# Optimization experiments

Measured on AMD Instinct MI355X. Metric: run time of the kernel, lower is better.

The kernel has to match this reference:

```python
import jax, jax.numpy as jnp
import numpy as np

K = 8192   # codebook_size
D = 256    # latent_dim
COMMITMENT_COST = 0.25


def setup_inputs() -> dict:
    key = jax.random.key(0)
    kx, kw = jax.random.split(key)
    x = jax.random.normal(kx, (8, 4096, D), dtype=jnp.float32)
    # nn.init.uniform_(weight, -1/K, 1/K)
    weight = jax.random.uniform(kw, (K, D), dtype=jnp.float32,
                                minval=-1.0 / K, maxval=1.0 / K)
    return {"x": x, "weight": weight}


def reference(x, weight):
    sg = jax.lax.stop_gradient
    orig_shape = x.shape
    x_flat = x.reshape(-1, D)                      # [N, D]
    # squared euclidean distances; argmin identical to cdist argmin
    x_sq = jnp.sum(x_flat * x_flat, axis=-1, keepdims=True)      # [N, 1]
    w_sq = jnp.sum(weight * weight, axis=-1)                     # [K]
    dist2 = x_sq - 2.0 * (x_flat @ weight.T) + w_sq              # [N, K]
    indices = jnp.argmin(dist2, axis=1)                          # [N]
    quantized = jnp.take(weight, indices, axis=0).reshape(orig_shape)
    # eval / non-EMA branch of the torch module
    commitment_loss = jnp.mean((x - sg(quantized)) ** 2) * COMMITMENT_COST
    codebook_loss = jnp.mean((quantized - sg(x)) ** 2)
    total = commitment_loss + codebook_loss
    # straight-through estimator
    quantized_st = x + sg(quantized - x)
    indices_out = indices.reshape(orig_shape[:-1])
    return quantized_st, indices_out, commitment_loss, codebook_loss, total
```

## Files before the change

### kernel.cpp

```cpp
#include <hip/hip_runtime.h>

#define K_CB   8192
#define D_DIM  256
#define N_ROWS 32768
#define Q_ELEMS (N_ROWS * D_DIM)

#define M_FLAG 1.3e-4f
#define M_CAND 1.3e-4f
#define CAP    16

typedef __bf16 bf16x8 __attribute__((ext_vector_type(8)));
typedef float  f32x16 __attribute__((ext_vector_type(16)));

#define ASYNC_COPY16(gp, lp)                                              \
    __builtin_amdgcn_global_load_lds(                                     \
        (const __attribute__((address_space(1))) unsigned int*)(gp),      \
        (__attribute__((address_space(3))) unsigned int*)(lp), 16, 0, 0)


__device__ inline ushort f2bf(float f) {
    unsigned u = __float_as_uint(f);
    unsigned r = u + 0x7FFFu + ((u >> 16) & 1u);
    return (ushort)(r >> 16);
}

__device__ inline uint4 pack8(float4 a, float4 b) {
    uint4 o;
    o.x = (unsigned)f2bf(a.x) | ((unsigned)f2bf(a.y) << 16);
    o.y = (unsigned)f2bf(a.z) | ((unsigned)f2bf(a.w) << 16);
    o.z = (unsigned)f2bf(b.x) | ((unsigned)f2bf(b.y) << 16);
    o.w = (unsigned)f2bf(b.z) | ((unsigned)f2bf(b.w) << 16);
    return o;
}

__global__ void wsq_wbf_kernel(const float* __restrict__ w, float* __restrict__ wsq,
                               ushort* __restrict__ wbf) {
    int wave = threadIdx.x >> 6, lane = threadIdx.x & 63;
    int row = blockIdx.x * 4 + wave;
    float4 v = reinterpret_cast<const float4*>(w)[(size_t)row * 64 + lane];
    uint2 o;
    o.x = (unsigned)f2bf(-2.0f * v.x) | ((unsigned)f2bf(-2.0f * v.y) << 16);
    o.y = (unsigned)f2bf(-2.0f * v.z) | ((unsigned)f2bf(-2.0f * v.w) << 16);
    int c = row & 127, tile = row >> 7;
    int s = lane >> 1, hq = lane & 1;
    size_t dst = (size_t)tile * 65536 + (size_t)c * 512 + (size_t)((s ^ (c & 7)) * 16) + hq * 8;
    *reinterpret_cast<uint2*>((char*)wbf + dst) = o;
    double sq = (double)v.x * v.x + (double)v.y * v.y + (double)v.z * v.z + (double)v.w * v.w;
    #pragma unroll
    for (int off = 32; off > 0; off >>= 1) sq += __shfl_down(sq, off, 64);
    if (lane == 0) wsq[row] = (float)sq;
}

__global__ void sqx_kernel(const float* __restrict__ m, float* __restrict__ out) {
    int wave = threadIdx.x >> 6, lane = threadIdx.x & 63;
    int row = blockIdx.x * 4 + wave;
    float4 v = reinterpret_cast<const float4*>(m)[(size_t)row * 64 + lane];
    double s = (double)v.x * v.x + (double)v.y * v.y + (double)v.z * v.z + (double)v.w * v.w;
    #pragma unroll
    for (int off = 32; off > 0; off >>= 1) s += __shfl_down(s, off, 64);
    if (lane == 0) out[row] = (float)s;
}

__global__ __launch_bounds__(256, 2) void pass1_kernel(
        const float* __restrict__ x, const ushort* __restrict__ wbf,
        const float* __restrict__ wsq, float* __restrict__ idx_out,
        float* __restrict__ rowmin, int* __restrict__ flags,
        unsigned* __restrict__ flag_count, int* __restrict__ hard_flags,
        unsigned* __restrict__ hard_count, int* __restrict__ candcnt,
        int* __restrict__ cands) {
    __shared__ __align__(16) ushort wt[128 * 256];

    const int t = threadIdx.x;
    const int lane = t & 63, ln31 = lane & 31, h = lane >> 5;
    const int wv = t >> 6, rs = wv & 1, cs = wv >> 1;
    const int r0 = blockIdx.x * 64;

    const int arow = r0 + rs * 32 + ln31;
    const float4* xr = reinterpret_cast<const float4*>(x) + (size_t)arow * 64;
    bf16x8 afr[16];
    #pragma unroll
    for (int kk = 0; kk < 16; ++kk)
        afr[kk] = __builtin_bit_cast(bf16x8, pack8(xr[kk * 4 + h * 2], xr[kk * 4 + h * 2 + 1]));

    float b1[16], b2[16];
    #pragma unroll
    for (int r = 0; r < 16; ++r) { b1[r] = 3.4e38f; b2[r] = 3.4e38f; }

    const int col0 = cs * 64 + ln31, c70 = col0 & 7;
    const char* gW = (const char*)wbf + (size_t)wv * 16384 + (size_t)lane * 16;
    char* lW = (char*)wt + wv * 16384;

    for (int tile = 0; tile < 64; ++tile) {
        __syncthreads();
        const char* gt = gW + (size_t)tile * 65536;
        #pragma unroll
        for (int i = 0; i < 16; ++i)
            ASYNC_COPY16(gt + i * 1024, lW + i * 1024);
        __syncthreads();

        int kb = tile * 128 + col0;
        float wsk0 = wsq[kb], wsk1 = wsq[kb + 32];

        f32x16 acc0 = {0,0,0,0,0,0,0,0,0,0,0,0,0,0,0,0};
        f32x16 acc1 = {0,0,0,0,0,0,0,0,0,0,0,0,0,0,0,0};
        #pragma unroll
        for (int kk = 0; kk < 16; ++kk) {
            int s = kk * 2 + h;
            bf16x8 bf0 = *reinterpret_cast<const bf16x8*>(&wt[col0 * 256 + ((s ^ c70) * 8)]);
            bf16x8 bf1 = *reinterpret_cast<const bf16x8*>(&wt[(col0 + 32) * 256 + ((s ^ c70) * 8)]);
            acc0 = __builtin_amdgcn_mfma_f32_32x32x16_bf16(afr[kk], bf0, acc0, 0, 0, 0);
            acc1 = __builtin_amdgcn_mfma_f32_32x32x16_bf16(afr[kk], bf1, acc1, 0, 0, 0);
        }

        #pragma unroll
        for (int r = 0; r < 16; ++r) {
            float s0 = acc0[r] + wsk0;
            float p0 = __uint_as_float((__float_as_uint(s0) & 0xFFFFE000u) | (unsigned)kb);
            b2[r] = __builtin_amdgcn_fmed3f(p0, b1[r], b2[r]);
            b1[r] = fminf(p0, b1[r]);
            float s1 = acc1[r] + wsk1;
            float p1 = __uint_as_float((__float_as_uint(s1) & 0xFFFFE000u) | (unsigned)(kb + 32));
            b2[r] = __builtin_amdgcn_fmed3f(p1, b1[r], b2[r]);
            b1[r] = fminf(p1, b1[r]);
        }
    }

    __syncthreads();
    float* sb1 = reinterpret_cast<float*>(wt);
    float* sb2 = sb1 + 4160;
    #pragma unroll
    for (int r = 0; r < 16; ++r) {
        int rl = rs * 32 + (r & 3) + 8 * (r >> 2) + 4 * h;
        sb1[rl * 65 + cs * 32 + ln31] = b1[r];
        sb2[rl * 65 + cs * 32 + ln31] = b2[r];
    }
    __syncthreads();
    if (t < 64) {
        float B1 = 3.4e38f, B2 = 3.4e38f;
        for (int c = 0; c < 64; ++c) {
            float a1 = sb1[t * 65 + c], a2 = sb2[t * 65 + c];
            float nb2 = fminf(fmaxf(B1, a1), fminf(B2, a2));
            B1 = fminf(B1, a1);
            B2 = nb2;
        }
        int row = r0 + t;
        idx_out[row] = (float)(__float_as_uint(B1) & 0x1FFFu);
        rowmin[row]  = B1;
        int nc = 0;
        if (B2 - B1 <= M_FLAG) {
            unsigned pos = atomicAdd(flag_count, 1u);
            if (pos < N_ROWS) flags[pos] = row;
            float T = B1 + M_CAND;
            bool hard = false;
            for (int c = 0; c < 64; ++c) {
                float a1 = sb1[t * 65 + c];
                if (a1 <= T) {
                    if (nc < CAP) cands[row * CAP + nc] = (int)(__float_as_uint(a1) & 0x1FFFu);
                    ++nc;
                }
                if (sb2[t * 65 + c] <= T) hard = true;
            }
            if (nc > CAP) hard = true;
            if (hard) {
                nc = 0;
                unsigned hp = atomicAdd(hard_count, 1u);
                if (hp < N_ROWS) hard_flags[hp] = row;
            }
        }
        candcnt[row] = nc;
    }
}

__global__ __launch_bounds__(256, 2) void fixup_kernel(
        const float* __restrict__ x, const ushort* __restrict__ wbf,
        const float* __restrict__ wsq, const float* __restrict__ rowmin,
        const int* __restrict__ hard_flags, const unsigned* __restrict__ hard_count,
        int* __restrict__ candcnt, int* __restrict__ cands) {
    __shared__ __align__(16) ushort wt[128 * 256];
    __shared__ int   sh_rows[64];
    __shared__ float sh_thr[64];

    const int t = threadIdx.x;
    const int lane = t & 63, ln31 = lane & 31, h = lane >> 5;
    const int wv = t >> 6, rs = wv & 1, cs = wv >> 1;

    unsigned cu = hard_count[0];
    int cnt = cu > N_ROWS ? N_ROWS : (int)cu;
    int nunits = ((cnt + 63) >> 6) * 8;

    for (int u = blockIdx.x; u < nunits; u += 512) {
        int ksp  = u & 7;
        int base = (u >> 3) * 64;
        int nrows = cnt - base; if (nrows > 64) nrows = 64;

        __syncthreads();
        if (t < 64) {
            int valid = (t < nrows);
            int gr = hard_flags[base + (valid ? t : 0)];
            sh_rows[t] = gr;
            sh_thr[t]  = valid ? rowmin[gr] + M_CAND : -3.4e38f;
        }
        __syncthreads();

        int arow = sh_rows[rs * 32 + ln31];
        const float4* xr = reinterpret_cast<const float4*>(x) + (size_t)arow * 64;
        bf16x8 afr[16];
        #pragma unroll
        for (int kk = 0; kk < 16; ++kk)
            afr[kk] = __builtin_bit_cast(bf16x8, pack8(xr[kk * 4 + h * 2], xr[kk * 4 + h * 2 + 1]));
        float thr_r[16];
        int   rl_r[16];
        #pragma unroll
        for (int r = 0; r < 16; ++r) {
            rl_r[r]  = rs * 32 + (r & 3) + 8 * (r >> 2) + 4 * h;
            thr_r[r] = sh_thr[rl_r[r]];
        }

        const int col0 = cs * 64 + ln31, c70 = col0 & 7;
        char* lW = (char*)wt + wv * 16384;

        for (int tile = 0; tile < 8; ++tile) {
            int ct0 = ksp * 1024 + tile * 128;
            __syncthreads();
            const char* gt = (const char*)wbf + ((size_t)ct0 << 9)
                           + (size_t)wv * 16384 + (size_t)lane * 16;
            #pragma unroll
            for (int i = 0; i < 16; ++i)
                ASYNC_COPY16(gt + i * 1024, lW + i * 1024);
            __syncthreads();

            float wsk0 = wsq[ct0 + col0], wsk1 = wsq[ct0 + col0 + 32];
            f32x16 acc0 = {0,0,0,0,0,0,0,0,0,0,0,0,0,0,0,0};
            f32x16 acc1 = {0,0,0,0,0,0,0,0,0,0,0,0,0,0,0,0};
            #pragma unroll
            for (int kk = 0; kk < 16; ++kk) {
                int s = kk * 2 + h;
                bf16x8 bf0 = *reinterpret_cast<const bf16x8*>(&wt[col0 * 256 + ((s ^ c70) * 8)]);
                bf16x8 bf1 = *reinterpret_cast<const bf16x8*>(&wt[(col0 + 32) * 256 + ((s ^ c70) * 8)]);
                acc0 = __builtin_amdgcn_mfma_f32_32x32x16_bf16(afr[kk], bf0, acc0, 0, 0, 0);
                acc1 = __builtin_amdgcn_mfma_f32_32x32x16_bf16(afr[kk], bf1, acc1, 0, 0, 0);
            }
            #pragma unroll
            for (int r = 0; r < 16; ++r) {
                float s0 = acc0[r] + wsk0;
                if (s0 <= thr_r[r]) {
                    int grow = sh_rows[rl_r[r]];
                    int pos = atomicAdd(&candcnt[grow], 1);
                    if (pos < CAP) cands[grow * CAP + pos] = ct0 + col0;
                }
                float s1 = acc1[r] + wsk1;
                if (s1 <= thr_r[r]) {
                    int grow = sh_rows[rl_r[r]];
                    int pos = atomicAdd(&candcnt[grow], 1);
                    if (pos < CAP) cands[grow * CAP + pos] = ct0 + col0 + 32;
                }
            }
        }
    }
}

__global__ __launch_bounds__(256) void rescore_kernel(
        const float* __restrict__ x, const float* __restrict__ w,
        const float* __restrict__ wsq, const float* __restrict__ xsq,
        const int* __restrict__ flags, const unsigned* __restrict__ flag_count,
        const int* __restrict__ candcnt, const int* __restrict__ cands,
        float* __restrict__ idx_out) {
    int wid  = (blockIdx.x * 256 + threadIdx.x) >> 6;
    int lane = threadIdx.x & 63;
    unsigned cu = flag_count[0];
    int cnt = (cu > N_ROWS) ? N_ROWS : (int)cu;

    for (int fi = wid; fi < cnt; fi += 1024) {
        int row = flags[fi];
        float4 xv = reinterpret_cast<const float4*>(x)[(size_t)row * 64 + lane];
        float Xs = xsq[row];
        int nc = candcnt[row]; if (nc > CAP) nc = CAP;
        float bq = 3.4e38f; int bk = -1;
        for (int c = 0; c < nc; ++c) {
            int k = cands[row * CAP + c];
            float4 wv = reinterpret_cast<const float4*>(w)[(size_t)k * 64 + lane];
            double d = (double)xv.x * wv.x + (double)xv.y * wv.y
                     + (double)xv.z * wv.z + (double)xv.w * wv.w;
            #pragma unroll
            for (int off = 1; off < 64; off <<= 1) d += __shfl_xor(d, off, 64);
            float XW = (float)d;
            float t3 = fmaf(-2.0f, XW, Xs);
            float qv = t3 + wsq[k];
            if (qv < bq || (qv == bq && k < bk) || bk < 0) { bq = qv; bk = k; }
        }
        if (lane == 0 && bk >= 0) idx_out[row] = (float)bk;
    }
}

__global__ __launch_bounds__(256) void gather_loss_kernel(
        const float* __restrict__ x, const float* __restrict__ w,
        const float* __restrict__ idx_f, float* __restrict__ out_q,
        float* __restrict__ accum) {
    const int nf4 = Q_ELEMS / 4;
    float lsum = 0.0f;
    for (int e = blockIdx.x * blockDim.x + threadIdx.x; e < nf4;
         e += gridDim.x * blockDim.x) {
        int row = e >> 6, d4 = e & 63;
        int k = (int)idx_f[row];
        float4 xv = reinterpret_cast<const float4*>(x)[e];
        float4 qv = reinterpret_cast<const float4*>(w)[(size_t)k * 64 + d4];
        float4 ov;
        ov.x = xv.x + (qv.x - xv.x);
        ov.y = xv.y + (qv.y - xv.y);
        ov.z = xv.z + (qv.z - xv.z);
        ov.w = xv.w + (qv.w - xv.w);
        reinterpret_cast<float4*>(out_q)[e] = ov;
        float dx = xv.x - qv.x, dy = xv.y - qv.y, dz = xv.z - qv.z, dw = xv.w - qv.w;
        lsum += dx * dx + dy * dy + dz * dz + dw * dw;
    }
    #pragma unroll
    for (int off = 32; off > 0; off >>= 1) lsum += __shfl_down(lsum, off, 64);
    __shared__ float ssum[4];
    if ((threadIdx.x & 63) == 0) ssum[threadIdx.x >> 6] = lsum;
    __syncthreads();
    if (threadIdx.x == 0)
        atomicAdd(accum, ssum[0] + ssum[1] + ssum[2] + ssum[3]);
}

__global__ void finalize_kernel(const float* __restrict__ accum,
                                float* __restrict__ out_tail) {
    float mse = accum[0] / (float)Q_ELEMS;
    float commit = 0.25f * mse;
    out_tail[0] = commit;
    out_tail[1] = mse;
    out_tail[2] = commit + mse;
}

extern "C" void kernel_launch(void* const* d_in, const int* in_sizes, int n_in,
                              void* d_out, int out_size, void* d_ws, size_t ws_size,
                              hipStream_t stream) {
    const float* x = (const float*)d_in[0];
    const float* w = (const float*)d_in[1];
    float* out = (float*)d_out;

    char* ws = (char*)d_ws;
    float*    Wsq        = (float*)ws;
    float*    Xsq        = (float*)(ws + 32768);
    float*    Rmin       = (float*)(ws + 163840);
    float*    accum      = (float*)(ws + 294912);
    unsigned* flag_count = (unsigned*)(ws + 294916);
    unsigned* hard_count = (unsigned*)(ws + 294920);
    int*      flags      = (int*)(ws + 294924);
    int*      hard_flags = (int*)(ws + 425996);
    int*      candcnt    = (int*)(ws + 557068);
    int*      cands      = (int*)(ws + 688140);
    ushort*   Wbf        = (ushort*)(ws + 2785296);

    hipMemsetAsync(ws + 294912, 0, 12, stream);
    wsq_wbf_kernel<<<K_CB / 4, 256, 0, stream>>>(w, Wsq, Wbf);
    sqx_kernel<<<N_ROWS / 4, 256, 0, stream>>>(x, Xsq);
    pass1_kernel<<<N_ROWS / 64, 256, 0, stream>>>(x, Wbf, Wsq, out + Q_ELEMS,
                                                  Rmin, flags, flag_count,
                                                  hard_flags, hard_count,
                                                  candcnt, cands);
    fixup_kernel<<<512, 256, 0, stream>>>(x, Wbf, Wsq, Rmin, hard_flags, hard_count,
                                          candcnt, cands);
    rescore_kernel<<<256, 256, 0, stream>>>(x, w, Wsq, Xsq, flags, flag_count,
                                            candcnt, cands, out + Q_ELEMS);
    gather_loss_kernel<<<8192, 256, 0, stream>>>(x, w, out + Q_ELEMS, out, accum);
    finalize_kernel<<<1, 1, 0, stream>>>(accum, out + Q_ELEMS + N_ROWS);
}
```

Before: 413.5 us.

## Double-buffer codebook tiles in pass1 with k-major layout and larger row blocks

Reorganizes the bf16 codebook into 64-code k-major blocks via an LDS transpose, so the MFMA B-operand loads become contiguous without XOR swizzle. Pass1 now uses 512 threads covering 128 rows per block and double-buffers 64-code tiles with async global-to-LDS copies, keeping one barrier per iteration so loads overlap compute. The separate x-squared kernel is dropped and the norm is recomputed inside rescore for flagged rows only. Each wave now issues one MFMA per tile instead of two, which may reduce MFMA-level ILP.

```diff
diff --git a/kernel.cpp b/kernel.cpp
--- a/kernel.cpp
+++ b/kernel.cpp
@@ -33,47 +33,64 @@
     return o;
 }
 
-__global__ void wsq_wbf_kernel(const float* __restrict__ w, float* __restrict__ wsq,
-                               ushort* __restrict__ wbf) {
-    int wave = threadIdx.x >> 6, lane = threadIdx.x & 63;
-    int row = blockIdx.x * 4 + wave;
-    float4 v = reinterpret_cast<const float4*>(w)[(size_t)row * 64 + lane];
-    uint2 o;
-    o.x = (unsigned)f2bf(-2.0f * v.x) | ((unsigned)f2bf(-2.0f * v.y) << 16);
-    o.y = (unsigned)f2bf(-2.0f * v.z) | ((unsigned)f2bf(-2.0f * v.w) << 16);
-    int c = row & 127, tile = row >> 7;
-    int s = lane >> 1, hq = lane & 1;
-    size_t dst = (size_t)tile * 65536 + (size_t)c * 512 + (size_t)((s ^ (c & 7)) * 16) + hq * 8;
-    *reinterpret_cast<uint2*>((char*)wbf + dst) = o;
-    double sq = (double)v.x * v.x + (double)v.y * v.y + (double)v.z * v.z + (double)v.w * v.w;
-    #pragma unroll
-    for (int off = 32; off > 0; off >>= 1) sq += __shfl_down(sq, off, 64);
-    if (lane == 0) wsq[row] = (float)sq;
-}
-
-__global__ void sqx_kernel(const float* __restrict__ m, float* __restrict__ out) {
-    int wave = threadIdx.x >> 6, lane = threadIdx.x & 63;
-    int row = blockIdx.x * 4 + wave;
-    float4 v = reinterpret_cast<const float4*>(m)[(size_t)row * 64 + lane];
-    double s = (double)v.x * v.x + (double)v.y * v.y + (double)v.z * v.z + (double)v.w * v.w;
-    #pragma unroll
-    for (int off = 32; off > 0; off >>= 1) s += __shfl_down(s, off, 64);
-    if (lane == 0) out[row] = (float)s;
-}
-
-__global__ __launch_bounds__(256, 2) void pass1_kernel(
+__global__ __launch_bounds__(256) void wsq_wbf_kernel(const float* __restrict__ w,
+                                                      float* __restrict__ wsq,
+                                                      ushort* __restrict__ wbf) {
+    __shared__ __align__(16) ushort tile[64 * 256];
+    const int t = threadIdx.x;
+    const int kb = blockIdx.x;
+    const int wv = t >> 6, lane = t & 63;
+
+    const float4* wb = reinterpret_cast<const float4*>(w) + (size_t)kb * 4096;
+    #pragma unroll
+    for (int i = 0; i < 16; ++i) {
+        int j = i * 256 + t;
+        float4 v = wb[j];
+        int c = j >> 6, d4 = j & 63;
+        uint2 o;
+        o.x = (unsigned)f2bf(-2.0f * v.x) | ((unsigned)f2bf(-2.0f * v.y) << 16);
+        o.y = (unsigned)f2bf(-2.0f * v.z) | ((unsigned)f2bf(-2.0f * v.w) << 16);
+        *reinterpret_cast<uint2*>((char*)tile + (size_t)(d4 >> 1) * 1024 + c * 16 + (d4 & 1) * 8) = o;
+    }
+
+    for (int c = wv; c < 64; c += 4) {
+        float4 v = reinterpret_cast<const float4*>(w)[(size_t)(kb * 64 + c) * 64 + lane];
+        double sq = (double)v.x * v.x + (double)v.y * v.y + (double)v.z * v.z + (double)v.w * v.w;
+        #pragma unroll
+        for (int off = 32; off > 0; off >>= 1) sq += __shfl_down(sq, off, 64);
+        if (lane == 0) wsq[kb * 64 + c] = (float)sq;
+    }
+
+    __syncthreads();
+    const uint4* src = reinterpret_cast<const uint4*>(tile);
+    uint4* dst = reinterpret_cast<uint4*>((char*)wbf + (size_t)kb * 32768);
+    #pragma unroll
+    for (int j = 0; j < 8; ++j) dst[j * 256 + t] = src[j * 256 + t];
+}
+
+__global__ __launch_bounds__(512, 2) void pass1_kernel(
         const float* __restrict__ x, const ushort* __restrict__ wbf,
         const float* __restrict__ wsq, float* __restrict__ idx_out,
         float* __restrict__ rowmin, int* __restrict__ flags,
         unsigned* __restrict__ flag_count, int* __restrict__ hard_flags,
         unsigned* __restrict__ hard_count, int* __restrict__ candcnt,
         int* __restrict__ cands) {
-    __shared__ __align__(16) ushort wt[128 * 256];
+    __shared__ __align__(16) char smem[66560];
+    ushort* wt = reinterpret_cast<ushort*>(smem);
 
     const int t = threadIdx.x;
     const int lane = t & 63, ln31 = lane & 31, h = lane >> 5;
-    const int wv = t >> 6, rs = wv & 1, cs = wv >> 1;
-    const int r0 = blockIdx.x * 64;
+    const int wv = t >> 6;
+    const int rs = wv >> 1, cs = wv & 1;
+    const int colL = cs * 32 + ln31;
+    const int r0 = blockIdx.x * 128;
+
+    {
+        const char* g = (const char*)wbf + (size_t)wv * 4096 + (size_t)lane * 16;
+        char* l = (char*)wt + wv * 4096;
+        #pragma unroll
+        for (int i = 0; i < 4; ++i) ASYNC_COPY16(g + i * 1024, l + i * 1024);
+    }
 
     const int arow = r0 + rs * 32 + ln31;
     const float4* xr = reinterpret_cast<const float4*>(x) + (size_t)arow * 64;
@@ -86,56 +103,50 @@
     #pragma unroll
     for (int r = 0; r < 16; ++r) { b1[r] = 3.4e38f; b2[r] = 3.4e38f; }
 
-    const int col0 = cs * 64 + ln31, c70 = col0 & 7;
-    const char* gW = (const char*)wbf + (size_t)wv * 16384 + (size_t)lane * 16;
-    char* lW = (char*)wt + wv * 16384;
-
-    for (int tile = 0; tile < 64; ++tile) {
-        __syncthreads();
-        const char* gt = gW + (size_t)tile * 65536;
-        #pragma unroll
-        for (int i = 0; i < 16; ++i)
-            ASYNC_COPY16(gt + i * 1024, lW + i * 1024);
-        __syncthreads();
-
-        int kb = tile * 128 + col0;
-        float wsk0 = wsq[kb], wsk1 = wsq[kb + 32];
-
-        f32x16 acc0 = {0,0,0,0,0,0,0,0,0,0,0,0,0,0,0,0};
-        f32x16 acc1 = {0,0,0,0,0,0,0,0,0,0,0,0,0,0,0,0};
+    __syncthreads();
+
+    int cur = 0;
+    for (int it = 0; it < 128; ++it) {
+        float wsk = wsq[it * 64 + colL];
+        {
+            const char* g = (const char*)wbf + (size_t)((it + 1) & 127) * 32768
+                          + (size_t)wv * 4096 + (size_t)lane * 16;
+            char* l = (char*)wt + (cur ^ 1) * 32768 + wv * 4096;
+            #pragma unroll
+            for (int i = 0; i < 4; ++i) ASYNC_COPY16(g + i * 1024, l + i * 1024);
+        }
+
+        const ushort* bt = wt + cur * 16384;
+        f32x16 acc = {0,0,0,0,0,0,0,0,0,0,0,0,0,0,0,0};
         #pragma unroll
         for (int kk = 0; kk < 16; ++kk) {
-            int s = kk * 2 + h;
-            bf16x8 bf0 = *reinterpret_cast<const bf16x8*>(&wt[col0 * 256 + ((s ^ c70) * 8)]);
-            bf16x8 bf1 = *reinterpret_cast<const bf16x8*>(&wt[(col0 + 32) * 256 + ((s ^ c70) * 8)]);
-            acc0 = __builtin_amdgcn_mfma_f32_32x32x16_bf16(afr[kk], bf0, acc0, 0, 0, 0);
-            acc1 = __builtin_amdgcn_mfma_f32_32x32x16_bf16(afr[kk], bf1, acc1, 0, 0, 0);
-        }
-
+            bf16x8 bf = *reinterpret_cast<const bf16x8*>(&bt[(size_t)(kk * 2 + h) * 512 + colL * 8]);
+            acc = __builtin_amdgcn_mfma_f32_32x32x16_bf16(afr[kk], bf, acc, 0, 0, 0);
+        }
+
+        const int kb = it * 64 + colL;
         #pragma unroll
         for (int r = 0; r < 16; ++r) {
-            float s0 = acc0[r] + wsk0;
+            float s0 = acc[r] + wsk;
             float p0 = __uint_as_float((__float_as_uint(s0) & 0xFFFFE000u) | (unsigned)kb);
             b2[r] = __builtin_amdgcn_fmed3f(p0, b1[r], b2[r]);
             b1[r] = fminf(p0, b1[r]);
-            float s1 = acc1[r] + wsk1;
-            float p1 = __uint_as_float((__float_as_uint(s1) & 0xFFFFE000u) | (unsigned)(kb + 32));
-            b2[r] = __builtin_amdgcn_fmed3f(p1, b1[r], b2[r]);
-            b1[r] = fminf(p1, b1[r]);
-        }
-    }
-
-    __syncthreads();
-    float* sb1 = reinterpret_cast<float*>(wt);
-    float* sb2 = sb1 + 4160;
+        }
+
+        __syncthreads();
+        cur ^= 1;
+    }
+
+    float* sb1 = reinterpret_cast<float*>(smem);
+    float* sb2 = sb1 + 128 * 65;
     #pragma unroll
     for (int r = 0; r < 16; ++r) {
         int rl = rs * 32 + (r & 3) + 8 * (r >> 2) + 4 * h;
-        sb1[rl * 65 + cs * 32 + ln31] = b1[r];
-        sb2[rl * 65 + cs * 32 + ln31] = b2[r];
+        sb1[rl * 65 + colL] = b1[r];
+        sb2[rl * 65 + colL] = b2[r];
     }
     __syncthreads();
-    if (t < 64) {
+    if (t < 128) {
         float B1 = 3.4e38f, B2 = 3.4e38f;
         for (int c = 0; c < 64; ++c) {
             float a1 = sb1[t * 65 + c], a2 = sb2[t * 65 + c];
@@ -176,13 +187,14 @@
         const float* __restrict__ wsq, const float* __restrict__ rowmin,
         const int* __restrict__ hard_flags, const unsigned* __restrict__ hard_count,
         int* __restrict__ candcnt, int* __restrict__ cands) {
-    __shared__ __align__(16) ushort wt[128 * 256];
+    __shared__ __align__(16) ushort wt[64 * 256];
     __shared__ int   sh_rows[64];
     __shared__ float sh_thr[64];
 
     const int t = threadIdx.x;
     const int lane = t & 63, ln31 = lane & 31, h = lane >> 5;
     const int wv = t >> 6, rs = wv & 1, cs = wv >> 1;
+    const int colL = cs * 32 + ln31;
 
     unsigned cu = hard_count[0];
     int cnt = cu > N_ROWS ? N_ROWS : (int)cu;
@@ -216,43 +228,33 @@
             thr_r[r] = sh_thr[rl_r[r]];
         }
 
-        const int col0 = cs * 64 + ln31, c70 = col0 & 7;
-        char* lW = (char*)wt + wv * 16384;
-
-        for (int tile = 0; tile < 8; ++tile) {
-            int ct0 = ksp * 1024 + tile * 128;
+        for (int tb = 0; tb < 16; ++tb) {
+            int blk = ksp * 16 + tb;
             __syncthreads();
-            const char* gt = (const char*)wbf + ((size_t)ct0 << 9)
-                           + (size_t)wv * 16384 + (size_t)lane * 16;
-            #pragma unroll
-            for (int i = 0; i < 16; ++i)
-                ASYNC_COPY16(gt + i * 1024, lW + i * 1024);
+            {
+                const char* g = (const char*)wbf + (size_t)blk * 32768
+                              + (size_t)wv * 8192 + (size_t)lane * 16;
+                char* l = (char*)wt + wv * 8192;
+                #pragma unroll
+                for (int i = 0; i < 8; ++i) ASYNC_COPY16(g + i * 1024, l + i * 1024);
+            }
             __syncthreads();
 
-            float wsk0 = wsq[ct0 + col0], wsk1 = wsq[ct0 + col0 + 32];
-            f32x16 acc0 = {0,0,0,0,0,0,0,0,0,0,0,0,0,0,0,0};
-            f32x16 acc1 = {0,0,0,0,0,0,0,0,0,0,0,0,0,0,0,0};
+            int kcol = blk * 64 + colL;
+            float wsk = wsq[kcol];
+            f32x16 acc = {0,0,0,0,0,0,0,0,0,0,0,0,0,0,0,0};
             #pragma unroll
             for (int kk = 0; kk < 16; ++kk) {
-                int s = kk * 2 + h;
-                bf16x8 bf0 = *reinterpret_cast<const bf16x8*>(&wt[col0 * 256 + ((s ^ c70) * 8)]);
-                bf16x8 bf1 = *reinterpret_cast<const bf16x8*>(&wt[(col0 + 32) * 256 + ((s ^ c70) * 8)]);
-                acc0 = __builtin_amdgcn_mfma_f32_32x32x16_bf16(afr[kk], bf0, acc0, 0, 0, 0);
-                acc1 = __builtin_amdgcn_mfma_f32_32x32x16_bf16(afr[kk], bf1, acc1, 0, 0, 0);
+                bf16x8 bf = *reinterpret_cast<const bf16x8*>(&wt[(size_t)(kk * 2 + h) * 512 + colL * 8]);
+                acc = __builtin_amdgcn_mfma_f32_32x32x16_bf16(afr[kk], bf, acc, 0, 0, 0);
             }
             #pragma unroll
             for (int r = 0; r < 16; ++r) {
-                float s0 = acc0[r] + wsk0;
+                float s0 = acc[r] + wsk;
                 if (s0 <= thr_r[r]) {
                     int grow = sh_rows[rl_r[r]];
                     int pos = atomicAdd(&candcnt[grow], 1);
-                    if (pos < CAP) cands[grow * CAP + pos] = ct0 + col0;
-                }
-                float s1 = acc1[r] + wsk1;
-                if (s1 <= thr_r[r]) {
-                    int grow = sh_rows[rl_r[r]];
-                    int pos = atomicAdd(&candcnt[grow], 1);
-                    if (pos < CAP) cands[grow * CAP + pos] = ct0 + col0 + 32;
+                    if (pos < CAP) cands[grow * CAP + pos] = kcol;
                 }
             }
         }
@@ -261,7 +263,7 @@
 
 __global__ __launch_bounds__(256) void rescore_kernel(
         const float* __restrict__ x, const float* __restrict__ w,
-        const float* __restrict__ wsq, const float* __restrict__ xsq,
+        const float* __restrict__ wsq,
         const int* __restrict__ flags, const unsigned* __restrict__ flag_count,
         const int* __restrict__ candcnt, const int* __restrict__ cands,
         float* __restrict__ idx_out) {
@@ -273,7 +275,11 @@
     for (int fi = wid; fi < cnt; fi += 1024) {
         int row = flags[fi];
         float4 xv = reinterpret_cast<const float4*>(x)[(size_t)row * 64 + lane];
-        float Xs = xsq[row];
+        double xs = (double)xv.x * xv.x + (double)xv.y * xv.y
+                  + (double)xv.z * xv.z + (double)xv.w * xv.w;
+        #pragma unroll
+        for (int off = 1; off < 64; off <<= 1) xs += __shfl_xor(xs, off, 64);
+        float Xs = (float)xs;
         int nc = candcnt[row]; if (nc > CAP) nc = CAP;
         float bq = 3.4e38f; int bk = -1;
         for (int c = 0; c < nc; ++c) {
@@ -340,7 +346,6 @@
 
     char* ws = (char*)d_ws;
     float*    Wsq        = (float*)ws;
-    float*    Xsq        = (float*)(ws + 32768);
     float*    Rmin       = (float*)(ws + 163840);
     float*    accum      = (float*)(ws + 294912);
     unsigned* flag_count = (unsigned*)(ws + 294916);
@@ -352,15 +357,14 @@
     ushort*   Wbf        = (ushort*)(ws + 2785296);
 
     hipMemsetAsync(ws + 294912, 0, 12, stream);
-    wsq_wbf_kernel<<<K_CB / 4, 256, 0, stream>>>(w, Wsq, Wbf);
-    sqx_kernel<<<N_ROWS / 4, 256, 0, stream>>>(x, Xsq);
-    pass1_kernel<<<N_ROWS / 64, 256, 0, stream>>>(x, Wbf, Wsq, out + Q_ELEMS,
-                                                  Rmin, flags, flag_count,
-                                                  hard_flags, hard_count,
-                                                  candcnt, cands);
+    wsq_wbf_kernel<<<K_CB / 64, 256, 0, stream>>>(w, Wsq, Wbf);
+    pass1_kernel<<<N_ROWS / 128, 512, 0, stream>>>(x, Wbf, Wsq, out + Q_ELEMS,
+                                                   Rmin, flags, flag_count,
+                                                   hard_flags, hard_count,
+                                                   candcnt, cands);
     fixup_kernel<<<512, 256, 0, stream>>>(x, Wbf, Wsq, Rmin, hard_flags, hard_count,
                                           candcnt, cands);
-    rescore_kernel<<<256, 256, 0, stream>>>(x, w, Wsq, Xsq, flags, flag_count,
+    rescore_kernel<<<256, 256, 0, stream>>>(x, w, Wsq, flags, flag_count,
                                             candcnt, cands, out + Q_ELEMS);
     gather_loss_kernel<<<8192, 256, 0, stream>>>(x, w, out + Q_ELEMS, out, accum);
     finalize_kernel<<<1, 1, 0, stream>>>(accum, out + Q_ELEMS + N_ROWS);
```

Result: no change. 408.5 us (-1.2%).
